# Kernel tuning notes

Measured on AMD Instinct MI355X. Metric: run time of the kernel, lower is better.

Reference implementation:

```python
import jax, jax.numpy as jnp
import numpy as np

UB = 35.0      # per-coordinate upper bound
SUM = 150.0    # equality constraint sum(z) = 150
NEG_SLOPE = 0.2


def _qp_project_one(v):
    """Solve min_z 0.5||z||^2 - v^T z  s.t. 0<=z<=UB, sum(z)=SUM  (n=5).
    Solution: z_i = clip(v_i - nu, 0, UB) with nu s.t. sum(z)=SUM.
    Exact closed form via the piecewise-linear breakpoints of g(nu)=sum(clip(v-nu,0,UB)).
    This matches QPFunction(Q=I, p=x, G,h box, A,b simplex) with v = -x."""
    bp = jnp.concatenate([v, v - UB])              # [10] breakpoints of g(nu)
    bs = jnp.sort(bp)[::-1]                        # descending in nu; g nondecreasing
    mid = 0.5 * (bs[:-1] + bs[1:])                 # [9] segment midpoints
    free = (v[None, :] > mid[:, None]) & (v[None, :] < mid[:, None] + UB)
    upper = v[None, :] >= mid[:, None] + UB
    nfree = jnp.sum(free, axis=1)
    num = jnp.sum(jnp.where(free, v[None, :], 0.0), axis=1) + UB * jnp.sum(upper, axis=1) - SUM
    nu_cand = num / jnp.maximum(nfree, 1)
    valid = (nfree > 0) & (nu_cand <= bs[:-1] + 1e-6) & (nu_cand >= bs[1:] - 1e-6)
    nu = nu_cand[jnp.argmax(valid)]
    return jnp.clip(v - nu, 0.0, UB)


def setup_inputs() -> dict:
    key = jax.random.key(0)
    ks = jax.random.split(key, 7)
    B, S, A = 65536, 17, 5
    state = jax.random.normal(ks[0], (B, S), dtype=jnp.float32)
    W1 = jax.random.normal(ks[1], (400, S), dtype=jnp.float32) * 0.05
    b1 = jax.random.normal(ks[2], (400,), dtype=jnp.float32) * 0.05
    W2 = jax.random.normal(ks[3], (300, 400), dtype=jnp.float32) * 0.05
    b2 = jax.random.normal(ks[4], (300,), dtype=jnp.float32) * 0.05
    W3 = jax.random.normal(ks[5], (A, 300), dtype=jnp.float32) * 0.05
    b3 = jax.random.normal(ks[6], (A,), dtype=jnp.float32) * 0.05
    return {"state": state, "W1": W1, "b1": b1, "W2": W2, "b2": b2,
            "W3": W3, "b3": b3, "training": 0}


def reference(state, W1, b1, W2, b2, W3, b3, training):
    lrelu = lambda x: jax.nn.leaky_relu(x, NEG_SLOPE)
    a = lrelu(state @ W1.T + b1)
    a = lrelu(a @ W2.T + b2)
    scaled_a = lrelu(a @ W3.T + b3)            # [B, 5]
    # QPFunction is called with linear term p = scaled_a, so v = -scaled_a
    opt_a = jax.vmap(_qp_project_one)(-scaled_a)
    return opt_a
```

## Files before the change

kernel.cpp:

```cpp
#include <hip/hip_runtime.h>
#include <hip/hip_bf16.h>

typedef __bf16 bf16x8 __attribute__((ext_vector_type(8)));
typedef float  f32x4  __attribute__((ext_vector_type(4)));

#define UBV   35.0f
#define SUMC  150.0f

__device__ __forceinline__ float lrelu(float x) { return fmaxf(x, 0.2f * x); }

__device__ __forceinline__ unsigned pk8(float a, float b) {
    return ((unsigned)__builtin_amdgcn_cvt_pk_fp8_f32(a, b, 0, false)) & 0xffffu;
}
__device__ __forceinline__ long mk64(unsigned lo, unsigned hi) {
    return (long)(((unsigned long long)hi << 32) | (unsigned long long)lo);
}
__device__ __forceinline__ void async16(void* lds_uniform, const void* gsrc) {
    __builtin_amdgcn_global_load_lds(
        (__attribute__((address_space(1))) void*)(gsrc),
        (__attribute__((address_space(3))) void*)(lds_uniform),
        16, 0, 0);
}


__global__ void prep_kernel(const float* __restrict__ W1, const float* __restrict__ b1,
                            const float* __restrict__ W2, const float* __restrict__ b2,
                            const float* __restrict__ W3, const float* __restrict__ b3,
                            __bf16* __restrict__ w1p, uint2* __restrict__ w2p,
                            uint2* __restrict__ w3c)
{
    int idx = blockIdx.x * blockDim.x + threadIdx.x;
    if (idx < 1664) {
        int lane = idx & 63;
        int nt = idx >> 6;
        int c16 = lane & 15, g = lane >> 4;
        int kk = nt >> 1, hh = nt & 1;
        int kap = kk * 32 + (c16 >> 2) * 8 + hh * 4 + (c16 & 3);
        bf16x8 v;
        #pragma unroll
        for (int j = 0; j < 8; ++j) {
            int k = g * 8 + j;
            float x = 0.f;
            if (kap < 400) {
                if (k < 17) x = W1[kap * 17 + k];
                else if (k == 17) x = b1[kap];
            } else if (kap == 400) {
                if (k == 17) x = 1.0f;
            }
            v[j] = (__bf16)x;
        }
        *(bf16x8*)(w1p + idx * 8) = v;
    } else if (idx < 1664 + 16640) {
        int i2 = idx - 1664;
        int fg = i2 >> 6, lane = i2 & 63;
        int q = fg / 65, rem = fg % 65;
        int t = rem / 13, kt = rem % 13;
        int c16 = lane & 15, g = lane >> 4;
        int local = t * 16 + c16;
        int ff = q * 79 + local;
        float v[8];
        #pragma unroll
        for (int j = 0; j < 8; ++j) {
            int kap = kt * 32 + g * 8 + j;
            float x = 0.f;
            if (local == 79) {
                x = (kap == 400) ? 1.0f : 0.f;
            } else if (local < 79 && ff < 300) {
                if (kap < 400) x = W2[ff * 400 + kap];
                else if (kap == 400) x = b2[ff];
            }
            v[j] = x;
        }
        uint2 d;
        d.x = pk8(v[0], v[1]) | (pk8(v[2], v[3]) << 16);
        d.y = pk8(v[4], v[5]) | (pk8(v[6], v[7]) << 16);
        w2p[i2] = d;
    } else if (idx < 1664 + 16640 + 768) {
        int i3 = idx - 1664 - 16640;
        int fg = i3 >> 6, lane = i3 & 63;
        int q = fg / 3, k2 = fg % 3;
        int o = lane & 15, g = lane >> 4;
        float v[8];
        #pragma unroll
        for (int j = 0; j < 8; ++j) {
            int t2  = 2 * k2 + (j >> 2);
            int rho = g * 4 + (j & 3);
            int local = t2 * 16 + rho;
            float x = 0.f;
            if (o < 5 && t2 < 5) {
                if (local == 79) x = b3[o] * 0.25f;
                else if (local < 79 && q * 79 + local < 300)
                    x = W3[o * 300 + q * 79 + local];
            }
            v[j] = x;
        }
        uint2 d;
        d.x = pk8(v[0], v[1]) | (pk8(v[2], v[3]) << 16);
        d.y = pk8(v[4], v[5]) | (pk8(v[6], v[7]) << 16);
        w3c[i3] = d;
    }
}

__global__ __launch_bounds__(256, 4)
void actor_kernel(const float* __restrict__ state,
                  const __bf16* __restrict__ w1p,
                  const uint2* __restrict__ w2p,
                  const uint2* __restrict__ w3c,
                  float* __restrict__ out)
{
    __shared__ __align__(16) char s_mem[33280];

    const int tid = threadIdx.x;
    const int wid = tid >> 6;
    const int ln  = tid & 63;
    const int g   = ln >> 4, c16 = ln & 15;
    const int brow = blockIdx.x << 6;

    {
        char* lb = s_mem;
        const char* gb = (const char*)w1p;
        #pragma unroll
        for (int i = wid; i < 26; i += 4)
            async16(lb + i * 1024, gb + i * 1024 + ln * 16);
    }

    bf16x8 sb;
    {
        const float* sp = state + (brow + wid * 16 + c16) * 17;
        if (g == 0) {
            #pragma unroll
            for (int j = 0; j < 8; ++j) sb[j] = (__bf16)sp[j];
        } else if (g == 1) {
            #pragma unroll
            for (int j = 0; j < 8; ++j) sb[j] = (__bf16)sp[8 + j];
        } else if (g == 2) {
            sb[0] = (__bf16)sp[16];
            sb[1] = (__bf16)1.0f;
            #pragma unroll
            for (int j = 2; j < 8; ++j) sb[j] = (__bf16)0.f;
        } else {
            #pragma unroll
            for (int j = 0; j < 8; ++j) sb[j] = (__bf16)0.f;
        }
    }

    __syncthreads();

    long frv[13];
    #pragma unroll
    for (int kt = 0; kt < 13; ++kt) {
        bf16x8 we = *(const bf16x8*)(s_mem + ((2 * kt) * 64 + ln) * 16);
        bf16x8 wo = *(const bf16x8*)(s_mem + ((2 * kt + 1) * 64 + ln) * 16);
        f32x4 ae = {0.f, 0.f, 0.f, 0.f}, ao = {0.f, 0.f, 0.f, 0.f};
        ae = __builtin_amdgcn_mfma_f32_16x16x32_bf16(we, sb, ae, 0, 0, 0);
        ao = __builtin_amdgcn_mfma_f32_16x16x32_bf16(wo, sb, ao, 0, 0, 0);
        frv[kt] = mk64(
            pk8(lrelu(ae[0]), lrelu(ae[1])) | (pk8(lrelu(ae[2]), lrelu(ae[3])) << 16),
            pk8(lrelu(ao[0]), lrelu(ao[1])) | (pk8(lrelu(ao[2]), lrelu(ao[3])) << 16));
    }

    __syncthreads();

    f32x4 ccs = {0.f, 0.f, 0.f, 0.f};
    const long* gw3 = (const long*)w3c;

    #pragma unroll 1
    for (int q = 0; q < 4; ++q) {
        {
            char* lb = s_mem;
            const char* gb = (const char*)w2p + q * 33280;
            #pragma unroll
            for (int i = wid; i < 32; i += 4)
                async16(lb + i * 1024, gb + i * 1024 + ln * 16);
            if (tid < 64)
                *(uint2*)(s_mem + 32768 + tid * 8) =
                    *(const uint2*)(gb + 32768 + tid * 8);
        }
        long w3q0 = gw3[(q * 3 + 0) * 64 + ln];
        long w3q1 = gw3[(q * 3 + 1) * 64 + ln];
        long w3q2 = gw3[(q * 3 + 2) * 64 + ln];

        __syncthreads();

        const long* wq = (const long*)s_mem;
        f32x4 acc0 = {0.f,0.f,0.f,0.f}, acc1 = {0.f,0.f,0.f,0.f};
        f32x4 acc2 = {0.f,0.f,0.f,0.f}, acc3 = {0.f,0.f,0.f,0.f};
        f32x4 acc4 = {0.f,0.f,0.f,0.f};
        #pragma unroll
        for (int kt = 0; kt < 13; ++kt) {
            long f0 = wq[(0 * 13 + kt) * 64 + ln];
            long f1 = wq[(1 * 13 + kt) * 64 + ln];
            long f2 = wq[(2 * 13 + kt) * 64 + ln];
            long f3 = wq[(3 * 13 + kt) * 64 + ln];
            long f4 = wq[(4 * 13 + kt) * 64 + ln];
            acc0 = __builtin_amdgcn_mfma_f32_16x16x32_fp8_fp8(f0, frv[kt], acc0, 0, 0, 0);
            acc1 = __builtin_amdgcn_mfma_f32_16x16x32_fp8_fp8(f1, frv[kt], acc1, 0, 0, 0);
            acc2 = __builtin_amdgcn_mfma_f32_16x16x32_fp8_fp8(f2, frv[kt], acc2, 0, 0, 0);
            acc3 = __builtin_amdgcn_mfma_f32_16x16x32_fp8_fp8(f3, frv[kt], acc3, 0, 0, 0);
            acc4 = __builtin_amdgcn_mfma_f32_16x16x32_fp8_fp8(f4, frv[kt], acc4, 0, 0, 0);
        }
        unsigned dw0 = pk8(lrelu(acc0[0]), lrelu(acc0[1])) | (pk8(lrelu(acc0[2]), lrelu(acc0[3])) << 16);
        unsigned dw1 = pk8(lrelu(acc1[0]), lrelu(acc1[1])) | (pk8(lrelu(acc1[2]), lrelu(acc1[3])) << 16);
        unsigned dw2 = pk8(lrelu(acc2[0]), lrelu(acc2[1])) | (pk8(lrelu(acc2[2]), lrelu(acc2[3])) << 16);
        unsigned dw3 = pk8(lrelu(acc3[0]), lrelu(acc3[1])) | (pk8(lrelu(acc3[2]), lrelu(acc3[3])) << 16);
        unsigned dw4 = pk8(lrelu(acc4[0]), lrelu(acc4[1])) | (pk8(lrelu(acc4[2]), lrelu(acc4[3])) << 16);
        f32x4 cc = {0.f, 0.f, 0.f, 0.f};
        cc = __builtin_amdgcn_mfma_f32_16x16x32_fp8_fp8(w3q0, mk64(dw0, dw1), cc, 0, 0, 0);
        cc = __builtin_amdgcn_mfma_f32_16x16x32_fp8_fp8(w3q1, mk64(dw2, dw3), cc, 0, 0, 0);
        cc = __builtin_amdgcn_mfma_f32_16x16x32_fp8_fp8(w3q2, mk64(dw4, 0u),  cc, 0, 0, 0);
        ccs += cc;

        __syncthreads();
    }

    float v4all = __shfl_xor(ccs[0], 16);

    if (ln < 16) {
        float v[5];
        v[0] = -lrelu(ccs[0]); v[1] = -lrelu(ccs[1]);
        v[2] = -lrelu(ccs[2]); v[3] = -lrelu(ccs[3]);
        v[4] = -lrelu(v4all);

        float bp[10];
        #pragma unroll
        for (int i = 0; i < 5; ++i) { bp[i] = v[i]; bp[i + 5] = v[i] - UBV; }
        float blo = -1e30f, glo = 0.f;
        #pragma unroll
        for (int j = 0; j < 10; ++j) {
            float b = bp[j];
            float gsum = 0.f;
            #pragma unroll
            for (int i = 0; i < 5; ++i) {
                float zc = v[i] - b;
                zc = fminf(fmaxf(zc, 0.f), UBV);
                gsum += zc;
            }
            if (gsum >= SUMC && b > blo) { blo = b; glo = gsum; }
        }
        float bhi = 1e30f;
        #pragma unroll
        for (int j = 0; j < 10; ++j) {
            float b = bp[j];
            if (b > blo && b < bhi) bhi = b;
        }
        float mid = 0.5f * (blo + bhi);
        int nfree = 0;
        #pragma unroll
        for (int i = 0; i < 5; ++i)
            nfree += (v[i] > mid && v[i] < mid + UBV) ? 1 : 0;
        float nu = (nfree > 0) ? blo + (glo - SUMC) / (float)nfree : blo;

        int row = brow + wid * 16 + ln;
        #pragma unroll
        for (int o = 0; o < 5; ++o) {
            float zf = v[o] - nu;
            zf = fminf(fmaxf(zf, 0.f), UBV);
            out[row * 5 + o] = zf;
        }
    }
}

extern "C" void kernel_launch(void* const* d_in, const int* in_sizes, int n_in,
                              void* d_out, int out_size, void* d_ws, size_t ws_size,
                              hipStream_t stream) {
    const float* state = (const float*)d_in[0];
    const float* W1    = (const float*)d_in[1];
    const float* b1    = (const float*)d_in[2];
    const float* W2    = (const float*)d_in[3];
    const float* b2    = (const float*)d_in[4];
    const float* W3    = (const float*)d_in[5];
    const float* b3    = (const float*)d_in[6];
    float* out = (float*)d_out;

    char* base = (char*)d_ws;
    __bf16* w1p = (__bf16*)base;
    uint2*  w2p = (uint2*)(base + 26624);
    uint2*  w3c = (uint2*)(base + 26624 + 133120);

    const int total = 1664 + 16640 + 768;
    prep_kernel<<<(total + 255) / 256, 256, 0, stream>>>(W1, b1, W2, b2, W3, b3,
                                                         w1p, w2p, w3c);

    int B = in_sizes[0] / 17;
    actor_kernel<<<B / 64, 256, 0, stream>>>(state, w1p, w2p, w3c, out);
}
```

Baseline: 29.72 us.

## Process two row tiles per wave and double-buffer W2 chunks in LDS

Each block now handles 128 rows instead of 64. Every wave computes two 16-row tiles, so each W2 fragment read from LDS feeds twice as many MFMAs. The W2 chunk loads are double-buffered: the next chunk is prefetched asynchronously into the other LDS buffer while the current one is consumed, which removes one barrier per iteration. The trade-off is more registers (launch bounds relaxed to 1 block) and half as many blocks, which lowers occupancy and wave-level latency hiding.

```diff
diff --git a/kernel.cpp b/kernel.cpp
--- a/kernel.cpp
+++ b/kernel.cpp
@@ -101,91 +101,98 @@
     }
 }
 
-__global__ __launch_bounds__(256, 4)
+__global__ __launch_bounds__(256, 1)
 void actor_kernel(const float* __restrict__ state,
                   const __bf16* __restrict__ w1p,
                   const uint2* __restrict__ w2p,
                   const uint2* __restrict__ w3c,
                   float* __restrict__ out)
 {
-    __shared__ __align__(16) char s_mem[33280];
+    __shared__ __align__(16) char s_mem[2][33792];
 
     const int tid = threadIdx.x;
     const int wid = tid >> 6;
     const int ln  = tid & 63;
     const int g   = ln >> 4, c16 = ln & 15;
-    const int brow = blockIdx.x << 6;
+    const int brow = blockIdx.x << 7;
 
     {
-        char* lb = s_mem;
-        const char* gb = (const char*)w1p;
+        const char* gb1 = (const char*)w1p;
         #pragma unroll
         for (int i = wid; i < 26; i += 4)
-            async16(lb + i * 1024, gb + i * 1024 + ln * 16);
-    }
-
-    bf16x8 sb;
+            async16(&s_mem[0][0] + i * 1024, gb1 + i * 1024 + ln * 16);
+        const char* gb2 = (const char*)w2p;
+        #pragma unroll
+        for (int i = wid; i < 33; i += 4)
+            async16(&s_mem[1][0] + i * 1024, gb2 + i * 1024 + ln * 16);
+    }
+
+    bf16x8 sbA, sbB;
     {
-        const float* sp = state + (brow + wid * 16 + c16) * 17;
+        const float* spA = state + (brow + wid * 32 + c16) * 17;
+        const float* spB = spA + 16 * 17;
         if (g == 0) {
             #pragma unroll
-            for (int j = 0; j < 8; ++j) sb[j] = (__bf16)sp[j];
+            for (int j = 0; j < 8; ++j) { sbA[j] = (__bf16)spA[j]; sbB[j] = (__bf16)spB[j]; }
         } else if (g == 1) {
             #pragma unroll
-            for (int j = 0; j < 8; ++j) sb[j] = (__bf16)sp[8 + j];
+            for (int j = 0; j < 8; ++j) { sbA[j] = (__bf16)spA[8 + j]; sbB[j] = (__bf16)spB[8 + j]; }
         } else if (g == 2) {
-            sb[0] = (__bf16)sp[16];
-            sb[1] = (__bf16)1.0f;
-            #pragma unroll
-            for (int j = 2; j < 8; ++j) sb[j] = (__bf16)0.f;
+            sbA[0] = (__bf16)spA[16]; sbB[0] = (__bf16)spB[16];
+            sbA[1] = (__bf16)1.0f;    sbB[1] = (__bf16)1.0f;
+            #pragma unroll
+            for (int j = 2; j < 8; ++j) { sbA[j] = (__bf16)0.f; sbB[j] = (__bf16)0.f; }
         } else {
             #pragma unroll
-            for (int j = 0; j < 8; ++j) sb[j] = (__bf16)0.f;
+            for (int j = 0; j < 8; ++j) { sbA[j] = (__bf16)0.f; sbB[j] = (__bf16)0.f; }
         }
     }
 
     __syncthreads();
 
-    long frv[13];
+    long frvA[13], frvB[13];
     #pragma unroll
     for (int kt = 0; kt < 13; ++kt) {
-        bf16x8 we = *(const bf16x8*)(s_mem + ((2 * kt) * 64 + ln) * 16);
-        bf16x8 wo = *(const bf16x8*)(s_mem + ((2 * kt + 1) * 64 + ln) * 16);
-        f32x4 ae = {0.f, 0.f, 0.f, 0.f}, ao = {0.f, 0.f, 0.f, 0.f};
-        ae = __builtin_amdgcn_mfma_f32_16x16x32_bf16(we, sb, ae, 0, 0, 0);
-        ao = __builtin_amdgcn_mfma_f32_16x16x32_bf16(wo, sb, ao, 0, 0, 0);
-        frv[kt] = mk64(
-            pk8(lrelu(ae[0]), lrelu(ae[1])) | (pk8(lrelu(ae[2]), lrelu(ae[3])) << 16),
-            pk8(lrelu(ao[0]), lrelu(ao[1])) | (pk8(lrelu(ao[2]), lrelu(ao[3])) << 16));
+        bf16x8 we = *(const bf16x8*)(&s_mem[0][0] + ((2 * kt) * 64 + ln) * 16);
+        bf16x8 wo = *(const bf16x8*)(&s_mem[0][0] + ((2 * kt + 1) * 64 + ln) * 16);
+        f32x4 aeA = {0.f,0.f,0.f,0.f}, aoA = {0.f,0.f,0.f,0.f};
+        f32x4 aeB = {0.f,0.f,0.f,0.f}, aoB = {0.f,0.f,0.f,0.f};
+        aeA = __builtin_amdgcn_mfma_f32_16x16x32_bf16(we, sbA, aeA, 0, 0, 0);
+        aoA = __builtin_amdgcn_mfma_f32_16x16x32_bf16(wo, sbA, aoA, 0, 0, 0);
+        aeB = __builtin_amdgcn_mfma_f32_16x16x32_bf16(we, sbB, aeB, 0, 0, 0);
+        aoB = __builtin_amdgcn_mfma_f32_16x16x32_bf16(wo, sbB, aoB, 0, 0, 0);
+        frvA[kt] = mk64(
+            pk8(lrelu(aeA[0]), lrelu(aeA[1])) | (pk8(lrelu(aeA[2]), lrelu(aeA[3])) << 16),
+            pk8(lrelu(aoA[0]), lrelu(aoA[1])) | (pk8(lrelu(aoA[2]), lrelu(aoA[3])) << 16));
+        frvB[kt] = mk64(
+            pk8(lrelu(aeB[0]), lrelu(aeB[1])) | (pk8(lrelu(aeB[2]), lrelu(aeB[3])) << 16),
+            pk8(lrelu(aoB[0]), lrelu(aoB[1])) | (pk8(lrelu(aoB[2]), lrelu(aoB[3])) << 16));
     }
 
     __syncthreads();
 
-    f32x4 ccs = {0.f, 0.f, 0.f, 0.f};
+    f32x4 ccsA = {0.f, 0.f, 0.f, 0.f};
+    f32x4 ccsB = {0.f, 0.f, 0.f, 0.f};
     const long* gw3 = (const long*)w3c;
 
     #pragma unroll 1
     for (int q = 0; q < 4; ++q) {
-        {
-            char* lb = s_mem;
-            const char* gb = (const char*)w2p + q * 33280;
-            #pragma unroll
-            for (int i = wid; i < 32; i += 4)
+        if (q < 3) {
+            char* lb = &s_mem[q & 1][0];
+            const char* gb = (const char*)w2p + (q + 1) * 33280;
+            #pragma unroll
+            for (int i = wid; i < 33; i += 4)
                 async16(lb + i * 1024, gb + i * 1024 + ln * 16);
-            if (tid < 64)
-                *(uint2*)(s_mem + 32768 + tid * 8) =
-                    *(const uint2*)(gb + 32768 + tid * 8);
         }
         long w3q0 = gw3[(q * 3 + 0) * 64 + ln];
         long w3q1 = gw3[(q * 3 + 1) * 64 + ln];
         long w3q2 = gw3[(q * 3 + 2) * 64 + ln];
 
-        __syncthreads();
-
-        const long* wq = (const long*)s_mem;
-        f32x4 acc0 = {0.f,0.f,0.f,0.f}, acc1 = {0.f,0.f,0.f,0.f};
-        f32x4 acc2 = {0.f,0.f,0.f,0.f}, acc3 = {0.f,0.f,0.f,0.f};
-        f32x4 acc4 = {0.f,0.f,0.f,0.f};
+        const long* wq = (const long*)(&s_mem[(q & 1) ^ 1][0]);
+        f32x4 aA0 = {0.f,0.f,0.f,0.f}, aA1 = {0.f,0.f,0.f,0.f}, aA2 = {0.f,0.f,0.f,0.f};
+        f32x4 aA3 = {0.f,0.f,0.f,0.f}, aA4 = {0.f,0.f,0.f,0.f};
+        f32x4 aB0 = {0.f,0.f,0.f,0.f}, aB1 = {0.f,0.f,0.f,0.f}, aB2 = {0.f,0.f,0.f,0.f};
+        f32x4 aB3 = {0.f,0.f,0.f,0.f}, aB4 = {0.f,0.f,0.f,0.f};
         #pragma unroll
         for (int kt = 0; kt < 13; ++kt) {
             long f0 = wq[(0 * 13 + kt) * 64 + ln];
@@ -193,33 +200,61 @@
             long f2 = wq[(2 * 13 + kt) * 64 + ln];
             long f3 = wq[(3 * 13 + kt) * 64 + ln];
             long f4 = wq[(4 * 13 + kt) * 64 + ln];
-            acc0 = __builtin_amdgcn_mfma_f32_16x16x32_fp8_fp8(f0, frv[kt], acc0, 0, 0, 0);
-            acc1 = __builtin_amdgcn_mfma_f32_16x16x32_fp8_fp8(f1, frv[kt], acc1, 0, 0, 0);
-            acc2 = __builtin_amdgcn_mfma_f32_16x16x32_fp8_fp8(f2, frv[kt], acc2, 0, 0, 0);
-            acc3 = __builtin_amdgcn_mfma_f32_16x16x32_fp8_fp8(f3, frv[kt], acc3, 0, 0, 0);
-            acc4 = __builtin_amdgcn_mfma_f32_16x16x32_fp8_fp8(f4, frv[kt], acc4, 0, 0, 0);
-        }
-        unsigned dw0 = pk8(lrelu(acc0[0]), lrelu(acc0[1])) | (pk8(lrelu(acc0[2]), lrelu(acc0[3])) << 16);
-        unsigned dw1 = pk8(lrelu(acc1[0]), lrelu(acc1[1])) | (pk8(lrelu(acc1[2]), lrelu(acc1[3])) << 16);
-        unsigned dw2 = pk8(lrelu(acc2[0]), lrelu(acc2[1])) | (pk8(lrelu(acc2[2]), lrelu(acc2[3])) << 16);
-        unsigned dw3 = pk8(lrelu(acc3[0]), lrelu(acc3[1])) | (pk8(lrelu(acc3[2]), lrelu(acc3[3])) << 16);
-        unsigned dw4 = pk8(lrelu(acc4[0]), lrelu(acc4[1])) | (pk8(lrelu(acc4[2]), lrelu(acc4[3])) << 16);
-        f32x4 cc = {0.f, 0.f, 0.f, 0.f};
-        cc = __builtin_amdgcn_mfma_f32_16x16x32_fp8_fp8(w3q0, mk64(dw0, dw1), cc, 0, 0, 0);
-        cc = __builtin_amdgcn_mfma_f32_16x16x32_fp8_fp8(w3q1, mk64(dw2, dw3), cc, 0, 0, 0);
-        cc = __builtin_amdgcn_mfma_f32_16x16x32_fp8_fp8(w3q2, mk64(dw4, 0u),  cc, 0, 0, 0);
-        ccs += cc;
-
-        __syncthreads();
-    }
-
-    float v4all = __shfl_xor(ccs[0], 16);
-
-    if (ln < 16) {
+            aA0 = __builtin_amdgcn_mfma_f32_16x16x32_fp8_fp8(f0, frvA[kt], aA0, 0, 0, 0);
+            aB0 = __builtin_amdgcn_mfma_f32_16x16x32_fp8_fp8(f0, frvB[kt], aB0, 0, 0, 0);
+            aA1 = __builtin_amdgcn_mfma_f32_16x16x32_fp8_fp8(f1, frvA[kt], aA1, 0, 0, 0);
+            aB1 = __builtin_amdgcn_mfma_f32_16x16x32_fp8_fp8(f1, frvB[kt], aB1, 0, 0, 0);
+            aA2 = __builtin_amdgcn_mfma_f32_16x16x32_fp8_fp8(f2, frvA[kt], aA2, 0, 0, 0);
+            aB2 = __builtin_amdgcn_mfma_f32_16x16x32_fp8_fp8(f2, frvB[kt], aB2, 0, 0, 0);
+            aA3 = __builtin_amdgcn_mfma_f32_16x16x32_fp8_fp8(f3, frvA[kt], aA3, 0, 0, 0);
+            aB3 = __builtin_amdgcn_mfma_f32_16x16x32_fp8_fp8(f3, frvB[kt], aB3, 0, 0, 0);
+            aA4 = __builtin_amdgcn_mfma_f32_16x16x32_fp8_fp8(f4, frvA[kt], aA4, 0, 0, 0);
+            aB4 = __builtin_amdgcn_mfma_f32_16x16x32_fp8_fp8(f4, frvB[kt], aB4, 0, 0, 0);
+        }
+        {
+            unsigned d0 = pk8(lrelu(aA0[0]), lrelu(aA0[1])) | (pk8(lrelu(aA0[2]), lrelu(aA0[3])) << 16);
+            unsigned d1 = pk8(lrelu(aA1[0]), lrelu(aA1[1])) | (pk8(lrelu(aA1[2]), lrelu(aA1[3])) << 16);
+            unsigned d2 = pk8(lrelu(aA2[0]), lrelu(aA2[1])) | (pk8(lrelu(aA2[2]), lrelu(aA2[3])) << 16);
+            unsigned d3 = pk8(lrelu(aA3[0]), lrelu(aA3[1])) | (pk8(lrelu(aA3[2]), lrelu(aA3[3])) << 16);
+            unsigned d4 = pk8(lrelu(aA4[0]), lrelu(aA4[1])) | (pk8(lrelu(aA4[2]), lrelu(aA4[3])) << 16);
+            f32x4 cc = {0.f, 0.f, 0.f, 0.f};
+            cc = __builtin_amdgcn_mfma_f32_16x16x32_fp8_fp8(w3q0, mk64(d0, d1), cc, 0, 0, 0);
+            cc = __builtin_amdgcn_mfma_f32_16x16x32_fp8_fp8(w3q1, mk64(d2, d3), cc, 0, 0, 0);
+            cc = __builtin_amdgcn_mfma_f32_16x16x32_fp8_fp8(w3q2, mk64(d4, 0u),  cc, 0, 0, 0);
+            ccsA += cc;
+        }
+        {
+            unsigned d0 = pk8(lrelu(aB0[0]), lrelu(aB0[1])) | (pk8(lrelu(aB0[2]), lrelu(aB0[3])) << 16);
+            unsigned d1 = pk8(lrelu(aB1[0]), lrelu(aB1[1])) | (pk8(lrelu(aB1[2]), lrelu(aB1[3])) << 16);
+            unsigned d2 = pk8(lrelu(aB2[0]), lrelu(aB2[1])) | (pk8(lrelu(aB2[2]), lrelu(aB2[3])) << 16);
+            unsigned d3 = pk8(lrelu(aB3[0]), lrelu(aB3[1])) | (pk8(lrelu(aB3[2]), lrelu(aB3[3])) << 16);
+            unsigned d4 = pk8(lrelu(aB4[0]), lrelu(aB4[1])) | (pk8(lrelu(aB4[2]), lrelu(aB4[3])) << 16);
+            f32x4 cc = {0.f, 0.f, 0.f, 0.f};
+            cc = __builtin_amdgcn_mfma_f32_16x16x32_fp8_fp8(w3q0, mk64(d0, d1), cc, 0, 0, 0);
+            cc = __builtin_amdgcn_mfma_f32_16x16x32_fp8_fp8(w3q1, mk64(d2, d3), cc, 0, 0, 0);
+            cc = __builtin_amdgcn_mfma_f32_16x16x32_fp8_fp8(w3q2, mk64(d4, 0u),  cc, 0, 0, 0);
+            ccsB += cc;
+        }
+        if (q < 3) __syncthreads();
+    }
+
+    float tA4 = __shfl_xor(ccsA[0], 16);
+    float sB0 = __shfl_xor(ccsB[0], 16);
+    float sB1 = __shfl_xor(ccsB[1], 16);
+    float sB2 = __shfl_xor(ccsB[2], 16);
+    float sB3 = __shfl_xor(ccsB[3], 16);
+
+    if (ln < 32) {
         float v[5];
-        v[0] = -lrelu(ccs[0]); v[1] = -lrelu(ccs[1]);
-        v[2] = -lrelu(ccs[2]); v[3] = -lrelu(ccs[3]);
-        v[4] = -lrelu(v4all);
+        if (ln < 16) {
+            v[0] = -lrelu(ccsA[0]); v[1] = -lrelu(ccsA[1]);
+            v[2] = -lrelu(ccsA[2]); v[3] = -lrelu(ccsA[3]);
+            v[4] = -lrelu(tA4);
+        } else {
+            v[0] = -lrelu(sB0); v[1] = -lrelu(sB1);
+            v[2] = -lrelu(sB2); v[3] = -lrelu(sB3);
+            v[4] = -lrelu(ccsB[0]);
+        }
 
         float bp[10];
         #pragma unroll
@@ -250,7 +285,7 @@
             nfree += (v[i] > mid && v[i] < mid + UBV) ? 1 : 0;
         float nu = (nfree > 0) ? blo + (glo - SUMC) / (float)nfree : blo;
 
-        int row = brow + wid * 16 + ln;
+        int row = brow + wid * 32 + ln;
         #pragma unroll
         for (int o = 0; o < 5; ++o) {
             float zf = v[o] - nu;
@@ -282,5 +317,5 @@
                                                          w1p, w2p, w3c);
 
     int B = in_sizes[0] / 17;
-    actor_kernel<<<B / 64, 256, 0, stream>>>(state, w1p, w2p, w3c, out);
-}
+    actor_kernel<<<B / 128, 256, 0, stream>>>(state, w1p, w2p, w3c, out);
+}
```

Measured after the change: 29.96 us. No clear change (+0.8%).
